# Kernel optimization log

Measured on AMD Instinct MI355X. Metric: run time of the kernel, lower is better.

## Reference

```python
import jax, jax.numpy as jnp
import numpy as np
import math

B, T, D = 32, 1024, 512
K, H = 64, 4
KP = K // H
MLP = 4 * D


def setup_inputs() -> dict:
    key = jax.random.key(0)
    ks = jax.random.split(key, 8)
    return {
        "x": jax.random.normal(ks[0], (B, T, D), jnp.float32),
        "w_in": jax.random.normal(ks[1], (D, 2 * K), jnp.float32) / math.sqrt(D),
        "log_decay": jax.random.uniform(ks[2], (K,), jnp.float32, -3.0, -0.1),
        "frequency": jnp.linspace(0.0, 2.0 * math.pi * (1.0 - 1.0 / K), K, dtype=jnp.float32),
        "coupling": jnp.broadcast_to(jnp.eye(KP, dtype=jnp.float32), (H, KP, KP))
                    + 0.01 * jax.random.normal(ks[3], (H, KP, KP), jnp.float32) / math.sqrt(KP),
        "w_out": jax.random.normal(ks[4], (2 * K, D), jnp.float32) / math.sqrt(2 * K),
        "w_gate": jax.random.normal(ks[5], (D, D), jnp.float32) / math.sqrt(D),
        "b_gate": jnp.full((D,), -2.0, jnp.float32),
        "w1": jax.random.normal(ks[6], (D, MLP), jnp.float32) / math.sqrt(D),
        "b1": jnp.zeros((MLP,), jnp.float32),
        "w2": jax.random.normal(ks[7], (MLP, D), jnp.float32) / math.sqrt(MLP),
        "b2": jnp.zeros((D,), jnp.float32),
        "g1": jnp.ones((D,), jnp.float32),
        "bn1": jnp.zeros((D,), jnp.float32),
        "g2": jnp.ones((D,), jnp.float32),
        "bn2": jnp.zeros((D,), jnp.float32),
    }


def _ln(x, g, b):
    m = jnp.mean(x, axis=-1, keepdims=True)
    v = jnp.var(x, axis=-1, keepdims=True)
    return (x - m) * jax.lax.rsqrt(v + 1e-5) * g + b


def reference(x, w_in, log_decay, frequency, coupling, w_out, w_gate, b_gate,
              w1, b1, w2, b2, g1, bn1, g2, bn2):
    Bv, Tv, Dv = x.shape
    residual = x
    xn = _ln(x, g1, bn1)
    beta = xn @ w_in                                   # [B,T,2K]
    beta_r, beta_i = jnp.split(beta, 2, axis=-1)       # each [B,T,K]
    # eigenstate kernel: lambda_k^n = sigmoid(log_decay)^n * exp(i n freq)
    mag = jax.nn.sigmoid(log_decay)                    # [K]
    n = jnp.arange(Tv, dtype=x.dtype)
    mag_pow = mag[None, :] ** n[:, None]               # [T,K]
    phase = n[:, None] * frequency[None, :]            # [T,K]
    kernel = jax.lax.complex(mag_pow * jnp.cos(phase), mag_pow * jnp.sin(phase))
    beta_c = jax.lax.complex(beta_r, beta_i)           # [B,T,K] complex
    # zero-pad to 2T for linear (causal) convolution via FFT
    B_f = jnp.fft.fft(jnp.pad(beta_c, ((0, 0), (0, Tv), (0, 0))), axis=1)  # [B,2T,K]
    K_f = jnp.fft.fft(jnp.pad(kernel, ((0, Tv), (0, 0))), axis=0)          # [2T,K]
    c = jnp.fft.ifft(B_f * K_f[None], axis=1)[:, :Tv, :]                   # [B,T,K]
    c_r, c_i = jnp.real(c), jnp.imag(c)
    # per-head coupling: block-diagonal matmul over eigenstates
    nh, kp = coupling.shape[0], coupling.shape[1]
    c_rh = c_r.reshape(Bv, Tv, nh, kp)
    c_ih = c_i.reshape(Bv, Tv, nh, kp)
    c_r = jnp.einsum('hjk,bthk->bthj', coupling, c_rh).reshape(Bv, Tv, nh * kp)
    c_i = jnp.einsum('hjk,bthk->bthj', coupling, c_ih).reshape(Bv, Tv, nh * kp)
    eigenstates = jnp.concatenate([c_r, c_i], axis=-1)  # [B,T,2K]
    h = eigenstates @ w_out                             # [B,T,D]
    gate = jax.nn.sigmoid(xn @ w_gate + b_gate)
    x1 = residual + gate * h
    xn2 = _ln(x1, g2, bn2)
    mlp = jax.nn.silu(xn2 @ w1 + b1) @ w2 + b2
    out = x1 + mlp
    return out, eigenstates
```

## Files before the change

kernel.cpp:

```cpp
#include <hip/hip_runtime.h>
#include <math.h>
#include <stdint.h>

#define Bb   32
#define Tt   1024
#define Dd   512
#define Kk   64
#define K2   128
#define Hh   4
#define KP   16
#define MLPD 2048
#define Mrows (Bb * Tt)

#define CW 48
#define CT 64

typedef unsigned short ushort_t;
typedef __attribute__((ext_vector_type(8))) short short8;
typedef __attribute__((ext_vector_type(4))) float floatx4;

__device__ __forceinline__ float sigf(float x) { return 1.0f / (1.0f + __expf(-x)); }

__device__ __forceinline__ ushort_t f2bf(float f) {
    unsigned u = __float_as_uint(f);
    u += 0x7fffu + ((u >> 16) & 1u);
    return (ushort_t)(u >> 16);
}
__device__ __forceinline__ float bf2f(ushort_t h) {
    return __uint_as_float(((unsigned)h) << 16);
}

__device__ __forceinline__ void async16(const void* g, void* l) {
    __builtin_amdgcn_global_load_lds((const __attribute__((address_space(1))) void*)g,
                                     (__attribute__((address_space(3))) void*)l, 16, 0, 0);
}

__global__ __launch_bounds__(256) void ln_bf_kernel(const float* __restrict__ x,
                                                    const float* __restrict__ g,
                                                    const float* __restrict__ b,
                                                    ushort_t* __restrict__ o) {
    int row  = blockIdx.x * 4 + (threadIdx.x >> 6);
    int lane = threadIdx.x & 63;
    const float4* xr = (const float4*)(x + (size_t)row * Dd);
    float4 a = xr[lane];
    float4 c = xr[lane + 64];
    float s = a.x + a.y + a.z + a.w + c.x + c.y + c.z + c.w;
    float q = a.x * a.x + a.y * a.y + a.z * a.z + a.w * a.w
            + c.x * c.x + c.y * c.y + c.z * c.z + c.w * c.w;
#pragma unroll
    for (int m = 32; m > 0; m >>= 1) {
        s += __shfl_xor(s, m);
        q += __shfl_xor(q, m);
    }
    float mean = s * (1.0f / Dd);
    float var  = q * (1.0f / Dd) - mean * mean;
    float rs   = rsqrtf(var + 1e-5f);
    const float4* gg = (const float4*)g;
    const float4* bb = (const float4*)b;
    float4 g0 = gg[lane], g1 = gg[lane + 64];
    float4 b0 = bb[lane], b1 = bb[lane + 64];
    ushort4 r0, r1;
    r0.x = f2bf((a.x - mean) * rs * g0.x + b0.x);
    r0.y = f2bf((a.y - mean) * rs * g0.y + b0.y);
    r0.z = f2bf((a.z - mean) * rs * g0.z + b0.z);
    r0.w = f2bf((a.w - mean) * rs * g0.w + b0.w);
    r1.x = f2bf((c.x - mean) * rs * g1.x + b1.x);
    r1.y = f2bf((c.y - mean) * rs * g1.y + b1.y);
    r1.z = f2bf((c.z - mean) * rs * g1.z + b1.z);
    r1.w = f2bf((c.w - mean) * rs * g1.w + b1.w);
    ushort4* oo = (ushort4*)(o + (size_t)row * Dd);
    oo[lane]      = r0;
    oo[lane + 64] = r1;
}

__global__ __launch_bounds__(256) void convert_transpose(const float* __restrict__ in,
                                                         ushort_t* __restrict__ out,
                                                         int R, int C) {
    __shared__ float t[32][33];
    int bx = blockIdx.x * 32;
    int by = blockIdx.y * 32;
    int tc = threadIdx.x & 31, tr = threadIdx.x >> 5;
#pragma unroll
    for (int i = 0; i < 4; i++)
        t[tr + 8 * i][tc] = in[(size_t)(by + tr + 8 * i) * C + bx + tc];
    __syncthreads();
#pragma unroll
    for (int i = 0; i < 4; i++)
        out[(size_t)(bx + tr + 8 * i) * R + by + tc] = f2bf(t[tc][tr + 8 * i]);
}

__global__ void kern_precompute(const float* __restrict__ log_decay,
                                const float* __restrict__ freq,
                                float* __restrict__ kern) {
    int i = blockIdx.x * 256 + threadIdx.x;
    if (i >= CW * Kk) return;
    int d = i >> 6, k = i & 63;
    float mag = 1.0f / (1.0f + expf(-log_decay[k]));
    float mp  = powf(mag, (float)d);
    float ph  = (float)d * freq[k];
    kern[d * K2 + k]      = mp * cosf(ph);
    kern[d * K2 + 64 + k] = mp * sinf(ph);
}

__global__ __launch_bounds__(256) void conv_kernel(const float* __restrict__ beta,
                                                   const float* __restrict__ kern,
                                                   const float* __restrict__ coup,
                                                   float* __restrict__ eig,
                                                   ushort_t* __restrict__ eigb) {
    __shared__ float sBeta[CT + CW][K2];
    __shared__ float sCoup[Hh][KP][KP];
    int b   = blockIdx.y;
    int t0  = blockIdx.x * CT;
    int tid = threadIdx.x;
    for (int i = tid; i < Hh * KP * KP; i += 256) {
        int h = i >> 8, j = (i >> 4) & 15, kk = i & 15;
        sCoup[h][kk][j] = coup[i];
    }
    for (int i = tid; i < (CT + CW) * K2; i += 256) {
        int r = i >> 7, c = i & 127;
        int t = t0 - CW + r;
        sBeta[r][c] = (t >= 0) ? beta[((size_t)b * Tt + t) * K2 + c] : 0.0f;
    }
    __syncthreads();
    int k  = tid & 63;
    int ts = tid >> 6;
    float cr[16], ci[16];
#pragma unroll
    for (int i = 0; i < 16; i++) { cr[i] = 0.0f; ci[i] = 0.0f; }
    for (int d = 0; d < CW; d++) {
        float kr = kern[d * K2 + k];
        float ki = kern[d * K2 + 64 + k];
#pragma unroll
        for (int i = 0; i < 16; i++) {
            int r    = CW + ts + 4 * i - d;
            float br = sBeta[r][k];
            float bi = sBeta[r][64 + k];
            cr[i] += kr * br - ki * bi;
            ci[i] += kr * bi + ki * br;
        }
    }
    __syncthreads();
#pragma unroll
    for (int i = 0; i < 16; i++) {
        int tl = ts + 4 * i;
        sBeta[tl][k]      = cr[i];
        sBeta[tl][64 + k] = ci[i];
    }
    __syncthreads();
    int h = k >> 4, jj = k & 15;
#pragma unroll
    for (int i = 0; i < 16; i++) {
        int tl = ts + 4 * i;
        float er = 0.0f, ei = 0.0f;
#pragma unroll
        for (int kk = 0; kk < KP; kk++) {
            float w = sCoup[h][kk][jj];
            er += w * sBeta[tl][h * KP + kk];
            ei += w * sBeta[tl][64 + h * KP + kk];
        }
        size_t off = ((size_t)b * Tt + t0 + tl) * K2;
        eig[off + k]       = er;
        eig[off + 64 + k]  = ei;
        eigb[off + k]      = f2bf(er);
        eigb[off + 64 + k] = f2bf(ei);
    }
}

enum { EPI_BETA = 0, EPI_GATE, EPI_X1, EPI_SILU, EPI_OUT0, EPI_OUTA };

template <int EPI>
__global__ __launch_bounds__(256) void mfma_gemm(
    const ushort_t* __restrict__ A, const ushort_t* __restrict__ Bt,
    void* __restrict__ Cv, int K, int ldb, int ldc,
    const float* __restrict__ bias,
    const float* __restrict__ aux1, const ushort_t* __restrict__ aux2) {
    __shared__ __align__(16) char lds[16384];
    char* sA = lds;
    char* sB = lds + 8192;
    int tid  = threadIdx.x;
    int lane = tid & 63, w = tid >> 6;
    int bm = blockIdx.y * 128, bn = blockIdx.x * 128;
    int wm = (w >> 1) * 64, wn = (w & 1) * 64;

    const char* gA[2];
    const char* gB[2];
    char* lA[2];
    char* lB[2];
#pragma unroll
    for (int q = 0; q < 2; q++) {
        int c = 2 * w + q;
        int m = c * 16 + (lane >> 2);
        int g = ((lane & 3) - ((m >> 1) & 3)) & 3;
        gA[q] = (const char*)(A  + (size_t)(bm + m) * K   + g * 8);
        gB[q] = (const char*)(Bt + (size_t)(bn + m) * ldb + g * 8);
        lA[q] = sA + c * 1024;
        lB[q] = sB + c * 1024;
    }
    int aoff[4], boff[4];
#pragma unroll
    for (int i = 0; i < 4; i++) {
        int m = wm + i * 16 + (lane & 15);
        aoff[i] = m * 64 + ((((lane >> 4) + (m >> 1)) & 3) * 16);
        int n = wn + i * 16 + (lane & 15);
        boff[i] = n * 64 + ((((lane >> 4) + (n >> 1)) & 3) * 16);
    }
    floatx4 acc[4][4];
#pragma unroll
    for (int i = 0; i < 4; i++)
#pragma unroll
        for (int j = 0; j < 4; j++) acc[i][j] = (floatx4)0.0f;

    for (int k0 = 0; k0 < K; k0 += 32) {
        size_t kb = (size_t)k0 * 2;
        async16(gA[0] + kb, lA[0]);
        async16(gA[1] + kb, lA[1]);
        async16(gB[0] + kb, lB[0]);
        async16(gB[1] + kb, lB[1]);
        __syncthreads();
        short8 af[4], bfr[4];
#pragma unroll
        for (int i = 0; i < 4; i++) af[i]  = *(const short8*)(sA + aoff[i]);
#pragma unroll
        for (int j = 0; j < 4; j++) bfr[j] = *(const short8*)(sB + boff[j]);
#pragma unroll
        for (int i = 0; i < 4; i++)
#pragma unroll
            for (int j = 0; j < 4; j++)
                acc[i][j] = __builtin_amdgcn_mfma_f32_16x16x32_bf16(af[i], bfr[j], acc[i][j], 0, 0, 0);
        __syncthreads();
    }
    int rq = (lane >> 4) * 4;
    int cn = lane & 15;
#pragma unroll
    for (int i = 0; i < 4; i++) {
#pragma unroll
        for (int j = 0; j < 4; j++) {
            int col = bn + wn + j * 16 + cn;
#pragma unroll
            for (int r = 0; r < 4; r++) {
                int row    = bm + wm + i * 16 + rq + r;
                size_t off = (size_t)row * ldc + col;
                float v    = acc[i][j][r];
                if (EPI == EPI_BETA) {
                    ((float*)Cv)[off] = v;
                } else if (EPI == EPI_GATE) {
                    ((ushort_t*)Cv)[off] = f2bf(sigf(v + bias[col]));
                } else if (EPI == EPI_X1) {
                    ((float*)Cv)[off] = aux1[off] + bf2f(aux2[off]) * v;
                } else if (EPI == EPI_SILU) {
                    float t = v + bias[col];
                    ((ushort_t*)Cv)[off] = f2bf(t * sigf(t));
                } else if (EPI == EPI_OUT0) {
                    float* C = (float*)Cv;
                    C[off] = C[off] + v + bias[col];
                } else {
                    float* C = (float*)Cv;
                    C[off] += v;
                }
            }
        }
    }
}

extern "C" void kernel_launch(void* const* d_in, const int* in_sizes, int n_in,
                              void* d_out, int out_size, void* d_ws, size_t ws_size,
                              hipStream_t stream) {
    (void)in_sizes; (void)n_in; (void)out_size;
    const float* x         = (const float*)d_in[0];
    const float* w_in      = (const float*)d_in[1];
    const float* log_decay = (const float*)d_in[2];
    const float* frequency = (const float*)d_in[3];
    const float* coupling  = (const float*)d_in[4];
    const float* w_out     = (const float*)d_in[5];
    const float* w_gate    = (const float*)d_in[6];
    const float* b_gate    = (const float*)d_in[7];
    const float* w1        = (const float*)d_in[8];
    const float* b1        = (const float*)d_in[9];
    const float* w2        = (const float*)d_in[10];
    const float* b2        = (const float*)d_in[11];
    const float* g1        = (const float*)d_in[12];
    const float* bn1       = (const float*)d_in[13];
    const float* g2        = (const float*)d_in[14];
    const float* bn2       = (const float*)d_in[15];

    float* out = (float*)d_out;
    float* eig = (float*)d_out + (size_t)Mrows * Dd;

    char* ws = (char*)d_ws;
    ushort_t* xn     = (ushort_t*)(ws);
    ushort_t* xn2    = (ushort_t*)(ws + (32ull  << 20));
    float*    beta   = (float*)   (ws + (64ull  << 20));
    ushort_t* eigb   = (ushort_t*)(ws + (80ull  << 20));
    ushort_t* gateb  = (ushort_t*)(ws + (88ull  << 20));
    ushort_t* w_inT  = (ushort_t*)(ws + (120ull << 20));
    ushort_t* w_gateT= (ushort_t*)(ws + (121ull << 20));
    ushort_t* w_outT = (ushort_t*)(ws + (122ull << 20));
    ushort_t* w1T    = (ushort_t*)(ws + (123ull << 20));
    ushort_t* w2T    = (ushort_t*)(ws + (125ull << 20));
    float*    kern   = (float*)   (ws + (127ull << 20));

    size_t base = 128ull << 20;
    ushort_t* hid;
    int CC;
    if (ws_size >= base + ((size_t)Mrows * 2048 * 2)) { hid = (ushort_t*)(ws + base); CC = 2048; }
    else if (ws_size >= base + ((size_t)Mrows * 1024 * 2)) { hid = (ushort_t*)(ws + base); CC = 1024; }
    else { hid = (ushort_t*)ws; CC = 512; }
    int nch = MLPD / CC;

    dim3 blk(256);
    convert_transpose<<<dim3(K2 / 32, Dd / 32), blk, 0, stream>>>(w_in, w_inT, Dd, K2);
    convert_transpose<<<dim3(Dd / 32, Dd / 32), blk, 0, stream>>>(w_gate, w_gateT, Dd, Dd);
    convert_transpose<<<dim3(Dd / 32, K2 / 32), blk, 0, stream>>>(w_out, w_outT, K2, Dd);
    convert_transpose<<<dim3(MLPD / 32, Dd / 32), blk, 0, stream>>>(w1, w1T, Dd, MLPD);
    convert_transpose<<<dim3(Dd / 32, MLPD / 32), blk, 0, stream>>>(w2, w2T, MLPD, Dd);
    kern_precompute<<<dim3((CW * Kk + 255) / 256), blk, 0, stream>>>(log_decay, frequency, kern);

    ln_bf_kernel<<<dim3(Mrows / 4), blk, 0, stream>>>(x, g1, bn1, xn);
    mfma_gemm<EPI_BETA><<<dim3(K2 / 128, Mrows / 128), blk, 0, stream>>>(
        xn, w_inT, beta, Dd, Dd, K2, nullptr, nullptr, nullptr);
    mfma_gemm<EPI_GATE><<<dim3(Dd / 128, Mrows / 128), blk, 0, stream>>>(
        xn, w_gateT, gateb, Dd, Dd, Dd, b_gate, nullptr, nullptr);
    conv_kernel<<<dim3(Tt / CT, Bb), blk, 0, stream>>>(beta, kern, coupling, eig, eigb);
    mfma_gemm<EPI_X1><<<dim3(Dd / 128, Mrows / 128), blk, 0, stream>>>(
        eigb, w_outT, out, K2, K2, Dd, nullptr, x, gateb);
    ln_bf_kernel<<<dim3(Mrows / 4), blk, 0, stream>>>(out, g2, bn2, xn2);
    for (int c = 0; c < nch; c++) {
        mfma_gemm<EPI_SILU><<<dim3(CC / 128, Mrows / 128), blk, 0, stream>>>(
            xn2, w1T + (size_t)c * CC * Dd, hid, Dd, Dd, CC, b1 + (size_t)c * CC, nullptr, nullptr);
        if (c == 0) {
            mfma_gemm<EPI_OUT0><<<dim3(Dd / 128, Mrows / 128), blk, 0, stream>>>(
                hid, w2T + (size_t)c * CC, out, CC, MLPD, Dd, b2, nullptr, nullptr);
        } else {
            mfma_gemm<EPI_OUTA><<<dim3(Dd / 128, Mrows / 128), blk, 0, stream>>>(
                hid, w2T + (size_t)c * CC, out, CC, MLPD, Dd, nullptr, nullptr, nullptr);
        }
    }
}
```

Measured before the change: 624.7 us.

## Double-buffer GEMM LDS tiles and fuse beta and gate projections

```diff
diff --git a/kernel.cpp b/kernel.cpp
--- a/kernel.cpp
+++ b/kernel.cpp
@@ -166,17 +166,17 @@
     }
 }
 
-enum { EPI_BETA = 0, EPI_GATE, EPI_X1, EPI_SILU, EPI_OUT0, EPI_OUTA };
+enum { EPI_INCOMB = 0, EPI_X1, EPI_SILU, EPI_OUT0, EPI_OUTA };
+
+#define STG 16384
 
 template <int EPI>
 __global__ __launch_bounds__(256) void mfma_gemm(
     const ushort_t* __restrict__ A, const ushort_t* __restrict__ Bt,
-    void* __restrict__ Cv, int K, int ldb, int ldc,
+    void* __restrict__ Cv, void* __restrict__ Cv2, int K, int ldb, int ldc,
     const float* __restrict__ bias,
     const float* __restrict__ aux1, const ushort_t* __restrict__ aux2) {
-    __shared__ __align__(16) char lds[16384];
-    char* sA = lds;
-    char* sB = lds + 8192;
+    __shared__ __align__(16) char lds[2 * STG];
     int tid  = threadIdx.x;
     int lane = tid & 63, w = tid >> 6;
     int bm = blockIdx.y * 128, bn = blockIdx.x * 128;
@@ -184,8 +184,7 @@
 
     const char* gA[2];
     const char* gB[2];
-    char* lA[2];
-    char* lB[2];
+    int lofsA[2], lofsB[2];
 #pragma unroll
     for (int q = 0; q < 2; q++) {
         int c = 2 * w + q;
@@ -193,8 +192,8 @@
         int g = ((lane & 3) - ((m >> 1) & 3)) & 3;
         gA[q] = (const char*)(A  + (size_t)(bm + m) * K   + g * 8);
         gB[q] = (const char*)(Bt + (size_t)(bn + m) * ldb + g * 8);
-        lA[q] = sA + c * 1024;
-        lB[q] = sB + c * 1024;
+        lofsA[q] = c * 1024;
+        lofsB[q] = 8192 + c * 1024;
     }
     int aoff[4], boff[4];
 #pragma unroll
@@ -202,7 +201,7 @@
         int m = wm + i * 16 + (lane & 15);
         aoff[i] = m * 64 + ((((lane >> 4) + (m >> 1)) & 3) * 16);
         int n = wn + i * 16 + (lane & 15);
-        boff[i] = n * 64 + ((((lane >> 4) + (n >> 1)) & 3) * 16);
+        boff[i] = 8192 + n * 64 + ((((lane >> 4) + (n >> 1)) & 3) * 16);
     }
     floatx4 acc[4][4];
 #pragma unroll
@@ -210,24 +209,35 @@
 #pragma unroll
         for (int j = 0; j < 4; j++) acc[i][j] = (floatx4)0.0f;
 
+    async16(gA[0], lds + lofsA[0]);
+    async16(gA[1], lds + lofsA[1]);
+    async16(gB[0], lds + lofsB[0]);
+    async16(gB[1], lds + lofsB[1]);
+    __syncthreads();
+
+    int p = 0;
     for (int k0 = 0; k0 < K; k0 += 32) {
-        size_t kb = (size_t)k0 * 2;
-        async16(gA[0] + kb, lA[0]);
-        async16(gA[1] + kb, lA[1]);
-        async16(gB[0] + kb, lB[0]);
-        async16(gB[1] + kb, lB[1]);
-        __syncthreads();
+        if (k0 + 32 < K) {
+            size_t kb = (size_t)(k0 + 32) * 2;
+            char* d = lds + (p ^ 1) * STG;
+            async16(gA[0] + kb, d + lofsA[0]);
+            async16(gA[1] + kb, d + lofsA[1]);
+            async16(gB[0] + kb, d + lofsB[0]);
+            async16(gB[1] + kb, d + lofsB[1]);
+        }
+        const char* s = lds + p * STG;
         short8 af[4], bfr[4];
 #pragma unroll
-        for (int i = 0; i < 4; i++) af[i]  = *(const short8*)(sA + aoff[i]);
-#pragma unroll
-        for (int j = 0; j < 4; j++) bfr[j] = *(const short8*)(sB + boff[j]);
+        for (int i = 0; i < 4; i++) af[i]  = *(const short8*)(s + aoff[i]);
+#pragma unroll
+        for (int j = 0; j < 4; j++) bfr[j] = *(const short8*)(s + boff[j]);
 #pragma unroll
         for (int i = 0; i < 4; i++)
 #pragma unroll
             for (int j = 0; j < 4; j++)
                 acc[i][j] = __builtin_amdgcn_mfma_f32_16x16x32_bf16(af[i], bfr[j], acc[i][j], 0, 0, 0);
         __syncthreads();
+        p ^= 1;
     }
     int rq = (lane >> 4) * 4;
     int cn = lane & 15;
@@ -239,23 +249,28 @@
 #pragma unroll
             for (int r = 0; r < 4; r++) {
                 int row    = bm + wm + i * 16 + rq + r;
-                size_t off = (size_t)row * ldc + col;
                 float v    = acc[i][j][r];
-                if (EPI == EPI_BETA) {
-                    ((float*)Cv)[off] = v;
-                } else if (EPI == EPI_GATE) {
-                    ((ushort_t*)Cv)[off] = f2bf(sigf(v + bias[col]));
+                if (EPI == EPI_INCOMB) {
+                    if (blockIdx.x == 0) {
+                        ((float*)Cv)[(size_t)row * K2 + col] = v;
+                    } else {
+                        int gc = col - 128;
+                        ((ushort_t*)Cv2)[(size_t)row * Dd + gc] = f2bf(sigf(v + bias[gc]));
+                    }
                 } else if (EPI == EPI_X1) {
+                    size_t off = (size_t)row * ldc + col;
                     ((float*)Cv)[off] = aux1[off] + bf2f(aux2[off]) * v;
                 } else if (EPI == EPI_SILU) {
+                    size_t off = (size_t)row * ldc + col;
                     float t = v + bias[col];
                     ((ushort_t*)Cv)[off] = f2bf(t * sigf(t));
                 } else if (EPI == EPI_OUT0) {
+                    size_t off = (size_t)row * ldc + col;
                     float* C = (float*)Cv;
                     C[off] = C[off] + v + bias[col];
                 } else {
-                    float* C = (float*)Cv;
-                    C[off] += v;
+                    size_t off = (size_t)row * ldc + col;
+                    ((float*)Cv)[off] += v;
                 }
             }
         }
@@ -287,17 +302,16 @@
     float* eig = (float*)d_out + (size_t)Mrows * Dd;
 
     char* ws = (char*)d_ws;
-    ushort_t* xn     = (ushort_t*)(ws);
-    ushort_t* xn2    = (ushort_t*)(ws + (32ull  << 20));
-    float*    beta   = (float*)   (ws + (64ull  << 20));
-    ushort_t* eigb   = (ushort_t*)(ws + (80ull  << 20));
-    ushort_t* gateb  = (ushort_t*)(ws + (88ull  << 20));
-    ushort_t* w_inT  = (ushort_t*)(ws + (120ull << 20));
-    ushort_t* w_gateT= (ushort_t*)(ws + (121ull << 20));
-    ushort_t* w_outT = (ushort_t*)(ws + (122ull << 20));
-    ushort_t* w1T    = (ushort_t*)(ws + (123ull << 20));
-    ushort_t* w2T    = (ushort_t*)(ws + (125ull << 20));
-    float*    kern   = (float*)   (ws + (127ull << 20));
+    ushort_t* xn      = (ushort_t*)(ws);
+    ushort_t* xn2     = (ushort_t*)(ws + (32ull  << 20));
+    float*    beta    = (float*)   (ws + (64ull  << 20));
+    ushort_t* eigb    = (ushort_t*)(ws + (80ull  << 20));
+    ushort_t* gateb   = (ushort_t*)(ws + (88ull  << 20));
+    ushort_t* w_comb  = (ushort_t*)(ws + (120ull << 20));
+    ushort_t* w_outT  = (ushort_t*)(ws + (122ull << 20));
+    ushort_t* w1T     = (ushort_t*)(ws + (123ull << 20));
+    ushort_t* w2T     = (ushort_t*)(ws + (125ull << 20));
+    float*    kern    = (float*)   (ws + (127ull << 20));
 
     size_t base = 128ull << 20;
     ushort_t* hid;
@@ -308,31 +322,29 @@
     int nch = MLPD / CC;
 
     dim3 blk(256);
-    convert_transpose<<<dim3(K2 / 32, Dd / 32), blk, 0, stream>>>(w_in, w_inT, Dd, K2);
-    convert_transpose<<<dim3(Dd / 32, Dd / 32), blk, 0, stream>>>(w_gate, w_gateT, Dd, Dd);
+    convert_transpose<<<dim3(K2 / 32, Dd / 32), blk, 0, stream>>>(w_in, w_comb, Dd, K2);
+    convert_transpose<<<dim3(Dd / 32, Dd / 32), blk, 0, stream>>>(w_gate, w_comb + (size_t)K2 * Dd, Dd, Dd);
     convert_transpose<<<dim3(Dd / 32, K2 / 32), blk, 0, stream>>>(w_out, w_outT, K2, Dd);
     convert_transpose<<<dim3(MLPD / 32, Dd / 32), blk, 0, stream>>>(w1, w1T, Dd, MLPD);
     convert_transpose<<<dim3(Dd / 32, MLPD / 32), blk, 0, stream>>>(w2, w2T, MLPD, Dd);
     kern_precompute<<<dim3((CW * Kk + 255) / 256), blk, 0, stream>>>(log_decay, frequency, kern);
 
     ln_bf_kernel<<<dim3(Mrows / 4), blk, 0, stream>>>(x, g1, bn1, xn);
-    mfma_gemm<EPI_BETA><<<dim3(K2 / 128, Mrows / 128), blk, 0, stream>>>(
-        xn, w_inT, beta, Dd, Dd, K2, nullptr, nullptr, nullptr);
-    mfma_gemm<EPI_GATE><<<dim3(Dd / 128, Mrows / 128), blk, 0, stream>>>(
-        xn, w_gateT, gateb, Dd, Dd, Dd, b_gate, nullptr, nullptr);
+    mfma_gemm<EPI_INCOMB><<<dim3(640 / 128, Mrows / 128), blk, 0, stream>>>(
+        xn, w_comb, beta, gateb, Dd, Dd, 0, b_gate, nullptr, nullptr);
     conv_kernel<<<dim3(Tt / CT, Bb), blk, 0, stream>>>(beta, kern, coupling, eig, eigb);
     mfma_gemm<EPI_X1><<<dim3(Dd / 128, Mrows / 128), blk, 0, stream>>>(
-        eigb, w_outT, out, K2, K2, Dd, nullptr, x, gateb);
+        eigb, w_outT, out, nullptr, K2, K2, Dd, nullptr, x, gateb);
     ln_bf_kernel<<<dim3(Mrows / 4), blk, 0, stream>>>(out, g2, bn2, xn2);
     for (int c = 0; c < nch; c++) {
         mfma_gemm<EPI_SILU><<<dim3(CC / 128, Mrows / 128), blk, 0, stream>>>(
-            xn2, w1T + (size_t)c * CC * Dd, hid, Dd, Dd, CC, b1 + (size_t)c * CC, nullptr, nullptr);
+            xn2, w1T + (size_t)c * CC * Dd, hid, nullptr, Dd, Dd, CC, b1 + (size_t)c * CC, nullptr, nullptr);
         if (c == 0) {
             mfma_gemm<EPI_OUT0><<<dim3(Dd / 128, Mrows / 128), blk, 0, stream>>>(
-                hid, w2T + (size_t)c * CC, out, CC, MLPD, Dd, b2, nullptr, nullptr);
+                hid, w2T + (size_t)c * CC, out, nullptr, CC, MLPD, Dd, b2, nullptr, nullptr);
         } else {
             mfma_gemm<EPI_OUTA><<<dim3(Dd / 128, Mrows / 128), blk, 0, stream>>>(
-                hid, w2T + (size_t)c * CC, out, CC, MLPD, Dd, nullptr, nullptr, nullptr);
-        }
-    }
-}
+                hid, w2T + (size_t)c * CC, out, nullptr, CC, MLPD, Dd, nullptr, nullptr, nullptr);
+        }
+    }
+}
```

New measurement: 592.4 us. 1.05x faster.
